# Optimization experiments

Measured on AMD Instinct MI355X. Metric: run time of the kernel, lower is better.

## Reference

```python
import jax, jax.numpy as jnp
import numpy as np

B=8; C=2; H=256; W=64; PH=4; PW=4; HP=H//PH; WP=W//PW; N=HP*WP
HID=1024; NH=16; HD=HID//NH; DEPTH=8; FFN=int(int(HID*4)*2/3); TDIM=256; OUT=PH*PW*C
EPS=1e-6


def _rmsnorm(x, w):
    return x * jax.lax.rsqrt(jnp.mean(x*x, -1, keepdims=True) + EPS) * w


def _modulate(x, shift, scale):
    return x * (1.0 + scale[:, None, :]) + shift[:, None, :]


def _rotate_half(x):
    x1 = x[..., 0::2]
    x2 = x[..., 1::2]
    return jnp.stack([-x2, x1], axis=-1).reshape(x.shape)


def _rope_tables():
    # 2D axial RoPE (EVA VisionRotaryEmbeddingFast style), dim per axis = HD//2
    dim = HD // 2
    freqs = 1.0 / (10000.0 ** (np.arange(0, dim, 2, dtype=np.float32) / dim))
    fh = np.repeat(np.outer(np.arange(HP, dtype=np.float32), freqs), 2, axis=-1)  # [HP,dim]
    fw = np.repeat(np.outer(np.arange(WP, dtype=np.float32), freqs), 2, axis=-1)  # [WP,dim]
    f = np.concatenate([np.broadcast_to(fh[:, None, :], (HP, WP, dim)),
                        np.broadcast_to(fw[None, :, :], (HP, WP, dim))], -1).reshape(N, HD)
    return jnp.asarray(np.cos(f)), jnp.asarray(np.sin(f))


def _sincos_1d(dim, pos):
    omega = np.arange(dim // 2, dtype=np.float32) / (dim / 2.0)
    omega = 1.0 / 10000.0 ** omega
    out = np.einsum('n,d->nd', pos.reshape(-1).astype(np.float32), omega)
    return np.concatenate([np.sin(out), np.cos(out)], -1)


def _pos_embed():
    gw, gh = np.meshgrid(np.arange(WP), np.arange(HP))  # row-major (HP, WP) grids
    emb = np.concatenate([_sincos_1d(HID // 2, gw), _sincos_1d(HID // 2, gh)], -1)
    return jnp.asarray(emb, dtype=jnp.float32)  # [N, HID]


_COS, _SIN = _rope_tables()
_POS = _pos_embed()


def _timestep_emb(t):
    half = TDIM // 2
    freqs = jnp.exp(-jnp.log(jnp.float32(10000.0)) * jnp.arange(half, dtype=jnp.float32) / half)
    args = t[:, None] * freqs[None]
    return jnp.concatenate([jnp.cos(args), jnp.sin(args)], -1)


def setup_inputs() -> dict:
    key = jax.random.key(0)
    ks = iter(jax.random.split(key, 16))
    def w(shape, s=0.02):
        return jax.random.normal(next(ks), shape, dtype=jnp.float32) * s
    return {
        'x': jax.random.normal(next(ks), (B, C, H, W), dtype=jnp.float32),
        't': jax.random.uniform(next(ks), (B,), dtype=jnp.float32) * 1000.0,
        'patch_w': w((HID, C, PH, PW)), 'patch_b': jnp.zeros((HID,), jnp.float32),
        't_w': w((HID, TDIM)), 't_b': jnp.zeros((HID,), jnp.float32),
        'norm1_w': jnp.ones((DEPTH, HID), jnp.float32),
        'qkv_w': w((DEPTH, 3 * HID, HID)), 'qkv_b': jnp.zeros((DEPTH, 3 * HID), jnp.float32),
        'qn_w': jnp.ones((DEPTH, HD), jnp.float32), 'kn_w': jnp.ones((DEPTH, HD), jnp.float32),
        'proj_w': w((DEPTH, HID, HID)), 'proj_b': jnp.zeros((DEPTH, HID), jnp.float32),
        'norm2_w': jnp.ones((DEPTH, HID), jnp.float32),
        'w12_w': w((DEPTH, 2 * FFN, HID)), 'w12_b': jnp.zeros((DEPTH, 2 * FFN), jnp.float32),
        'w3_w': w((DEPTH, HID, FFN)), 'w3_b': jnp.zeros((DEPTH, HID), jnp.float32),
        'ada_w': w((DEPTH, 6 * HID, HID)), 'ada_b': jnp.zeros((DEPTH, 6 * HID), jnp.float32),
        'fnorm_w': jnp.ones((HID,), jnp.float32),
        'flin_w': w((OUT, HID)), 'flin_b': jnp.zeros((OUT,), jnp.float32),
        'fada_w': w((2 * HID, HID)), 'fada_b': jnp.zeros((2 * HID,), jnp.float32),
    }


def reference(x, t, patch_w, patch_b, t_w, t_b, norm1_w, qkv_w, qkv_b, qn_w, kn_w,
              proj_w, proj_b, norm2_w, w12_w, w12_b, w3_w, w3_b, ada_w, ada_b,
              fnorm_w, flin_w, flin_b, fada_w, fada_b):
    # timestep embedding -> c : [B, HID]
    c = _timestep_emb(t) @ t_w.T + t_b
    cs = jax.nn.silu(c)
    # patch embed (conv stride==kernel == patchify + matmul)
    xp = x.reshape(B, C, HP, PH, WP, PW)
    h = jnp.einsum('bchpwq,ocpq->bhwo', xp, patch_w).reshape(B, N, HID) + patch_b
    h = h + _POS[None]
    scale = 1.0 / np.sqrt(HD)
    for d in range(DEPTH):
        ada = cs @ ada_w[d].T + ada_b[d]
        sm, scm, gm, sp, scp, gp = jnp.split(ada, 6, axis=-1)
        hn = _modulate(_rmsnorm(h, norm1_w[d]), sm, scm)
        qkv = (hn @ qkv_w[d].T + qkv_b[d]).reshape(B, N, 3, NH, HD).transpose(2, 0, 3, 1, 4)
        q, k, v = qkv[0], qkv[1], qkv[2]  # [B, NH, N, HD]
        q = _rmsnorm(q, qn_w[d]) 
        k = _rmsnorm(k, kn_w[d])
        q = q * _COS + _rotate_half(q) * _SIN
        k = k * _COS + _rotate_half(k) * _SIN
        attn = jax.nn.softmax(jnp.einsum('bhqd,bhkd->bhqk', q, k) * scale, axis=-1)
        o = jnp.einsum('bhqk,bhkd->bqhd', attn, v).reshape(B, N, HID)
        o = o @ proj_w[d].T + proj_b[d]
        h = h + gm[:, None, :] * o
        hn = _modulate(_rmsnorm(h, norm2_w[d]), sp, scp)
        x12 = hn @ w12_w[d].T + w12_b[d]
        x1, x2 = jnp.split(x12, 2, axis=-1)
        h = h + gp[:, None, :] * ((jax.nn.silu(x1) * x2) @ w3_w[d].T + w3_b[d])
    fsh, fsc = jnp.split(cs @ fada_w.T + fada_b, 2, axis=-1)
    h = _modulate(_rmsnorm(h, fnorm_w), fsh, fsc) @ flin_w.T + flin_b  # [B, N, OUT]
    y = h.reshape(B, HP, WP, PH, PW, C)
    return jnp.einsum('nhwpqc->nchpwq', y).reshape(B, C, H, W)
```

## Files before the change

### kernel.cpp

```cpp
#include <hip/hip_runtime.h>
#include <stdint.h>

typedef __bf16 bf16;
typedef __attribute__((ext_vector_type(8))) __bf16 bf16x8;
typedef __attribute__((ext_vector_type(4))) float floatx4;

#define NTOK   1024
#define TOKS   8192
#define HID_   1024
#define FFN_   2730
#define FFNP   2752
#define X12N   5460

#define EPI_BF16  0
#define EPI_QKV   1
#define EPI_RESID 2

__global__ __launch_bounds__(256) void conv_bf16(const float* __restrict__ in, bf16* __restrict__ out, int n)
{
    const int i = (blockIdx.x * 256 + threadIdx.x) * 4;
    if (i >= n) return;
    const float4 v = *(const float4*)(in + i);
    out[i + 0] = (bf16)v.x; out[i + 1] = (bf16)v.y;
    out[i + 2] = (bf16)v.z; out[i + 3] = (bf16)v.w;
}

__global__ void conv_pad_w3(const float* __restrict__ w3, bf16* __restrict__ w3p)
{
    const int kk = blockIdx.x * 256 + threadIdx.x;
    const int row = blockIdx.y;
    if (kk >= FFNP) return;
    w3p[(size_t)row * FFNP + kk] = (kk < FFN_) ? (bf16)w3[(size_t)row * FFN_ + kk] : (bf16)0.f;
}

__global__ __launch_bounds__(256) void gemm_bt(
    const bf16* __restrict__ A, const bf16* __restrict__ Bm, const float* __restrict__ bias,
    int K, int Nreal, int epi,
    bf16* __restrict__ outb, int ldo,
    bf16* __restrict__ qo, bf16* __restrict__ ko, bf16* __restrict__ vo,
    float* __restrict__ hres, const float* __restrict__ gate, int gstride)
{
    __shared__ __align__(16) bf16 As[128 * 32];
    __shared__ __align__(16) bf16 Bs[128 * 32];
    const int t    = threadIdx.x;
    const int M0   = blockIdx.y * 128;
    const int N0   = blockIdx.x * 128;
    const int lane = t & 63;
    const int w    = t >> 6;
    const int wr   = (w >> 1) * 64, wc = (w & 1) * 64;
    const int quad = lane >> 4, r16 = lane & 15;
    const int sr   = t >> 2;
    const int sk   = (t & 3) * 8;
    const int Nlast = Nreal - 1;

    floatx4 acc[4][4];
    const floatx4 zero = {0.f, 0.f, 0.f, 0.f};
    #pragma unroll
    for (int i = 0; i < 4; i++)
        #pragma unroll
        for (int j = 0; j < 4; j++) acc[i][j] = zero;

    for (int k0 = 0; k0 < K; k0 += 32) {
        const bf16* ga0 = A + (size_t)(M0 + sr) * K + k0 + sk;
        const bf16* ga1 = A + (size_t)(M0 + sr + 64) * K + k0 + sk;
        int n0c = N0 + sr;      if (n0c > Nlast) n0c = Nlast;
        int n1c = N0 + sr + 64; if (n1c > Nlast) n1c = Nlast;
        const bf16* gb0 = Bm + (size_t)n0c * K + k0 + sk;
        const bf16* gb1 = Bm + (size_t)n1c * K + k0 + sk;
        __builtin_amdgcn_global_load_lds((const __attribute__((address_space(1))) void*)ga0,
            (__attribute__((address_space(3))) void*)(As + t * 8), 16, 0, 0);
        __builtin_amdgcn_global_load_lds((const __attribute__((address_space(1))) void*)ga1,
            (__attribute__((address_space(3))) void*)(As + (t + 256) * 8), 16, 0, 0);
        __builtin_amdgcn_global_load_lds((const __attribute__((address_space(1))) void*)gb0,
            (__attribute__((address_space(3))) void*)(Bs + t * 8), 16, 0, 0);
        __builtin_amdgcn_global_load_lds((const __attribute__((address_space(1))) void*)gb1,
            (__attribute__((address_space(3))) void*)(Bs + (t + 256) * 8), 16, 0, 0);
        __syncthreads();
        bf16x8 af[4], bfv[4];
        #pragma unroll
        for (int i = 0; i < 4; i++) af[i]  = *(const bf16x8*)(As + (wr + i * 16 + r16) * 32 + quad * 8);
        #pragma unroll
        for (int j = 0; j < 4; j++) bfv[j] = *(const bf16x8*)(Bs + (wc + j * 16 + r16) * 32 + quad * 8);
        #pragma unroll
        for (int i = 0; i < 4; i++)
            #pragma unroll
            for (int j = 0; j < 4; j++)
                acc[i][j] = __builtin_amdgcn_mfma_f32_16x16x32_bf16(af[i], bfv[j], acc[i][j], 0, 0, 0);
        __syncthreads();
    }

    #pragma unroll
    for (int i = 0; i < 4; i++) {
        const int rbase = M0 + wr + i * 16 + quad * 4;
        #pragma unroll
        for (int j = 0; j < 4; j++) {
            const int col = N0 + wc + j * 16 + r16;
            if (col >= Nreal) continue;
            const float bv = bias[col];
            if (epi == EPI_BF16) {
                #pragma unroll
                for (int rr = 0; rr < 4; rr++) {
                    const int row = rbase + rr;
                    outb[(size_t)row * ldo + col] = (bf16)(acc[i][j][rr] + bv);
                }
            } else if (epi == EPI_QKV) {
                const int s = col >> 10, hh = (col >> 6) & 15, dd = col & 63;
                #pragma unroll
                for (int rr = 0; rr < 4; rr++) {
                    const int row = rbase + rr;
                    const int b = row >> 10, n = row & 1023;
                    const float vv = acc[i][j][rr] + bv;
                    if (s == 0)      qo[((size_t)(b * 16 + hh) * 1024 + n) * 64 + dd] = (bf16)vv;
                    else if (s == 1) ko[((size_t)(b * 16 + hh) * 1024 + n) * 64 + dd] = (bf16)vv;
                    else             vo[((size_t)(b * 16 + hh) * 64 + dd) * 1024 + n] = (bf16)vv;
                }
            } else {
                #pragma unroll
                for (int rr = 0; rr < 4; rr++) {
                    const int row = rbase + rr;
                    const int b = row >> 10;
                    hres[(size_t)row * 1024 + col] += gate[(size_t)b * gstride + col] * (acc[i][j][rr] + bv);
                }
            }
        }
    }
}

__global__ __launch_bounds__(256) void small_gemm(
    const float* __restrict__ Aws, const float* __restrict__ t_in,
    const float* __restrict__ W, const float* __restrict__ bias,
    float* __restrict__ out, int N, int K, int mode, int dosilu)
{
    const int w = threadIdx.x >> 6, lane = threadIdx.x & 63;
    const int col = blockIdx.x * 4 + w;
    float acc[8];
    #pragma unroll
    for (int bb = 0; bb < 8; bb++) acc[bb] = 0.f;
    float tb[8];
    if (mode == 1) {
        #pragma unroll
        for (int bb = 0; bb < 8; bb++) tb[bb] = t_in[bb];
    }
    for (int kk = lane; kk < K; kk += 64) {
        const float wv = W[(size_t)col * K + kk];
        if (mode == 1) {
            const float f = __expf(-(float)(kk & 127) * (9.21034037198f / 128.f));
            #pragma unroll
            for (int bb = 0; bb < 8; bb++) {
                const float arg = tb[bb] * f;
                const float e = (kk < 128) ? cosf(arg) : sinf(arg);
                acc[bb] += e * wv;
            }
        } else {
            #pragma unroll
            for (int bb = 0; bb < 8; bb++) acc[bb] += Aws[(size_t)bb * 1024 + kk] * wv;
        }
    }
    #pragma unroll
    for (int bb = 0; bb < 8; bb++) {
        float v2 = acc[bb];
        #pragma unroll
        for (int off = 32; off; off >>= 1) v2 += __shfl_xor(v2, off, 64);
        acc[bb] = v2;
    }
    if (lane == 0) {
        const float bv = bias[col];
        #pragma unroll
        for (int bb = 0; bb < 8; bb++) {
            float vv = acc[bb] + bv;
            if (dosilu) vv = vv / (1.f + __expf(-vv));
            out[(size_t)bb * N + col] = vv;
        }
    }
}

__global__ __launch_bounds__(256) void patch_embed(
    const float* __restrict__ x, const float* __restrict__ pw, const float* __restrict__ pb,
    float* __restrict__ h)
{
    __shared__ float xs[32];
    const int row = blockIdx.x, t = threadIdx.x;
    const int b = row >> 10, n = row & 1023;
    const int hp = n >> 4, wp = n & 15;
    if (t < 32) {
        const int c = t >> 4, ph = (t >> 2) & 3, pq = t & 3;
        xs[t] = x[((size_t)(b * 2 + c) * 256 + hp * 4 + ph) * 64 + wp * 4 + pq];
    }
    __syncthreads();
    #pragma unroll
    for (int rep = 0; rep < 4; rep++) {
        const int o = t + rep * 256;
        const float* wrow = pw + (size_t)o * 32;
        float acc = pb[o];
        #pragma unroll
        for (int e = 0; e < 32; e++) acc += xs[e] * wrow[e];
        const int seg = o >> 8, oo = o & 255;
        const float om = __expf(-(float)oo * (9.21034037198f / 256.f));
        const float pos = (seg < 2) ? (float)wp : (float)hp;
        const float arg = pos * om;
        const float pe = ((seg & 1) == 0) ? sinf(arg) : cosf(arg);
        h[(size_t)row * 1024 + o] = acc + pe;
    }
}

__global__ __launch_bounds__(256) void norm_mod(
    const float* __restrict__ h, const float* __restrict__ w,
    const float* __restrict__ ada, int sh_off, int sc_off, int stride,
    bf16* __restrict__ out)
{
    __shared__ float red[4];
    const int row = blockIdx.x, t = threadIdx.x;
    const int b = row >> 10;
    const float4 xv = ((const float4*)(h + (size_t)row * 1024))[t];
    float ss = xv.x * xv.x + xv.y * xv.y + xv.z * xv.z + xv.w * xv.w;
    #pragma unroll
    for (int off = 32; off; off >>= 1) ss += __shfl_xor(ss, off, 64);
    if ((t & 63) == 0) red[t >> 6] = ss;
    __syncthreads();
    const float total = red[0] + red[1] + red[2] + red[3];
    const float rms = rsqrtf(total * (1.f / 1024.f) + 1e-6f);
    const float* sh = ada + (size_t)b * stride + sh_off;
    const float* sc = ada + (size_t)b * stride + sc_off;
    const float vals[4] = {xv.x, xv.y, xv.z, xv.w};
    #pragma unroll
    for (int e = 0; e < 4; e++) {
        const int c2 = t * 4 + e;
        const float vv = vals[e] * rms * w[c2] * (1.f + sc[c2]) + sh[c2];
        out[(size_t)row * 1024 + c2] = (bf16)vv;
    }
}

__global__ __launch_bounds__(64) void rope_qk(
    bf16* __restrict__ q, bf16* __restrict__ k,
    const float* __restrict__ qw, const float* __restrict__ kw)
{
    const int n = blockIdx.x, bh = blockIdx.y, d = threadIdx.x;
    const size_t idx = ((size_t)bh * 1024 + n) * 64 + d;
    const float qv = (float)q[idx], kv = (float)k[idx];
    float sq = qv * qv, sk = kv * kv;
    #pragma unroll
    for (int off = 32; off; off >>= 1) { sq += __shfl_xor(sq, off, 64); sk += __shfl_xor(sk, off, 64); }
    const float rq = rsqrtf(sq * (1.f / 64.f) + 1e-6f);
    const float rk = rsqrtf(sk * (1.f / 64.f) + 1e-6f);
    const float qn = qv * rq * qw[d];
    const float kn = kv * rk * kw[d];
    const int j = (d & 31) >> 1;
    const float freq = __expf(-(float)j * (9.21034037198f / 16.f));
    const float pos = (d < 32) ? (float)(n >> 4) : (float)(n & 15);
    const float ang = pos * freq;
    const float cv = cosf(ang), sv = sinf(ang);
    const float qp = __shfl_xor(qn, 1, 64);
    const float kp = __shfl_xor(kn, 1, 64);
    const float qo = qn * cv + ((d & 1) ? qp : -qp) * sv;
    const float ko = kn * cv + ((d & 1) ? kp : -kp) * sv;
    q[idx] = (bf16)qo;
    k[idx] = (bf16)ko;
}

__global__ __launch_bounds__(256) void attn_kernel(
    const bf16* __restrict__ q, const bf16* __restrict__ k, const bf16* __restrict__ v,
    bf16* __restrict__ o)
{
    __shared__ __align__(16) bf16 Qs[2 * 64 * 32];
    __shared__ __align__(16) bf16 Ks[2 * 64 * 32];
    __shared__ __align__(16) bf16 Vt[2 * 64 * 32];
    __shared__ __align__(16) bf16 Pw[4 * 16 * 80];
    const int t = threadIdx.x;
    const int l = t & 63, wq = t >> 6;
    const int quad = l >> 4, r16 = l & 15;
    const int qt = blockIdx.x, bh = blockIdx.y;
    const int b = bh >> 4, hh = bh & 15;

    #pragma unroll
    for (int m = 0; m < 2; m++) {
        const bf16* g = q + ((size_t)bh * 1024 + qt * 64 + wq * 16 + (l >> 2)) * 64 + m * 32 + (l & 3) * 8;
        __builtin_amdgcn_global_load_lds((const __attribute__((address_space(1))) void*)g,
            (__attribute__((address_space(3))) void*)(Qs + m * 2048 + wq * 16 * 32 + l * 8), 16, 0, 0);
    }
    __syncthreads();
    bf16x8 afq[2];
    #pragma unroll
    for (int h2 = 0; h2 < 2; h2++)
        afq[h2] = *(const bf16x8*)(Qs + h2 * 2048 + (wq * 16 + r16) * 32 + quad * 8);

    float m_r[4], l_r[4];
    floatx4 oacc[4];
    const floatx4 zero = {0.f, 0.f, 0.f, 0.f};
    #pragma unroll
    for (int rr = 0; rr < 4; rr++) { m_r[rr] = -1e30f; l_r[rr] = 0.f; }
    #pragma unroll
    for (int jd = 0; jd < 4; jd++) oacc[jd] = zero;

    bf16* Pme = Pw + wq * 16 * 80;

    for (int kt = 0; kt < 16; kt++) {
        __syncthreads();
        #pragma unroll
        for (int m = 0; m < 2; m++) {
            const bf16* gk = k + ((size_t)bh * 1024 + kt * 64 + wq * 16 + (l >> 2)) * 64 + m * 32 + (l & 3) * 8;
            __builtin_amdgcn_global_load_lds((const __attribute__((address_space(1))) void*)gk,
                (__attribute__((address_space(3))) void*)(Ks + m * 2048 + wq * 16 * 32 + l * 8), 16, 0, 0);
            const bf16* gv = v + ((size_t)bh * 64 + wq * 16 + (l >> 2)) * 1024 + kt * 64 + m * 32 + (l & 3) * 8;
            __builtin_amdgcn_global_load_lds((const __attribute__((address_space(1))) void*)gv,
                (__attribute__((address_space(3))) void*)(Vt + m * 2048 + wq * 16 * 32 + l * 8), 16, 0, 0);
        }
        __syncthreads();

        floatx4 s[4];
        #pragma unroll
        for (int j = 0; j < 4; j++) {
            bf16x8 b0 = *(const bf16x8*)(Ks + 0 * 2048 + (j * 16 + r16) * 32 + quad * 8);
            bf16x8 b1 = *(const bf16x8*)(Ks + 1 * 2048 + (j * 16 + r16) * 32 + quad * 8);
            s[j] = __builtin_amdgcn_mfma_f32_16x16x32_bf16(afq[0], b0, zero, 0, 0, 0);
            s[j] = __builtin_amdgcn_mfma_f32_16x16x32_bf16(afq[1], b1, s[j], 0, 0, 0);
        }
        float alpha[4];
        #pragma unroll
        for (int rr = 0; rr < 4; rr++) {
            float mx = fmaxf(fmaxf(s[0][rr], s[1][rr]), fmaxf(s[2][rr], s[3][rr])) * 0.125f;
            #pragma unroll
            for (int off2 = 1; off2 < 16; off2 <<= 1) mx = fmaxf(mx, __shfl_xor(mx, off2, 64));
            const float mn = fmaxf(m_r[rr], mx);
            float ps = 0.f;
            #pragma unroll
            for (int j = 0; j < 4; j++) {
                const float e = __expf(s[j][rr] * 0.125f - mn);
                s[j][rr] = e; ps += e;
            }
            #pragma unroll
            for (int off2 = 1; off2 < 16; off2 <<= 1) ps += __shfl_xor(ps, off2, 64);
            alpha[rr] = __expf(m_r[rr] - mn);
            l_r[rr] = l_r[rr] * alpha[rr] + ps;
            m_r[rr] = mn;
        }
        #pragma unroll
        for (int j = 0; j < 4; j++)
            #pragma unroll
            for (int rr = 0; rr < 4; rr++)
                Pme[(quad * 4 + rr) * 80 + j * 16 + r16] = (bf16)s[j][rr];
        __asm__ volatile("s_waitcnt lgkmcnt(0)" ::: "memory");
        bf16x8 afp[2];
        #pragma unroll
        for (int st = 0; st < 2; st++)
            afp[st] = *(const bf16x8*)(Pme + r16 * 80 + st * 32 + quad * 8);
        #pragma unroll
        for (int jd = 0; jd < 4; jd++)
            #pragma unroll
            for (int rr = 0; rr < 4; rr++) oacc[jd][rr] *= alpha[rr];
        #pragma unroll
        for (int jd = 0; jd < 4; jd++) {
            bf16x8 b0 = *(const bf16x8*)(Vt + 0 * 2048 + (jd * 16 + r16) * 32 + quad * 8);
            bf16x8 b1 = *(const bf16x8*)(Vt + 1 * 2048 + (jd * 16 + r16) * 32 + quad * 8);
            oacc[jd] = __builtin_amdgcn_mfma_f32_16x16x32_bf16(afp[0], b0, oacc[jd], 0, 0, 0);
            oacc[jd] = __builtin_amdgcn_mfma_f32_16x16x32_bf16(afp[1], b1, oacc[jd], 0, 0, 0);
        }
    }
    #pragma unroll
    for (int rr = 0; rr < 4; rr++) {
        const float inv = 1.f / l_r[rr];
        const size_t base = ((size_t)b * 1024 + qt * 64 + wq * 16 + quad * 4 + rr) * 1024 + hh * 64;
        #pragma unroll
        for (int jd = 0; jd < 4; jd++)
            o[base + jd * 16 + r16] = (bf16)(oacc[jd][rr] * inv);
    }
}

__global__ void swiglu_kernel(const bf16* __restrict__ x12, bf16* __restrict__ g)
{
    const int kk = blockIdx.x * 256 + threadIdx.x;
    const int row = blockIdx.y;
    if (kk >= FFNP) return;
    float gv = 0.f;
    if (kk < FFN_) {
        const float a  = (float)x12[(size_t)row * X12N + kk];
        const float b2 = (float)x12[(size_t)row * X12N + FFN_ + kk];
        gv = a * b2 / (1.f + __expf(-a));
    }
    g[(size_t)row * FFNP + kk] = (bf16)gv;
}

__global__ __launch_bounds__(256) void final_head(
    const bf16* __restrict__ hn, const float* __restrict__ fw, const float* __restrict__ fb,
    float* __restrict__ out)
{
    __shared__ float hs[1024];
    const int row = blockIdx.x, t = threadIdx.x;
    #pragma unroll
    for (int r = 0; r < 4; r++) hs[t + r * 256] = (float)hn[(size_t)row * 1024 + t + r * 256];
    __syncthreads();
    const int o = t >> 3, s = t & 7;
    float acc = 0.f;
    const float* wr = fw + (size_t)o * 1024 + s * 128;
    const float* hb = hs + s * 128;
    for (int e = 0; e < 128; e++) acc += hb[e] * wr[e];
    #pragma unroll
    for (int off = 1; off < 8; off <<= 1) acc += __shfl_xor(acc, off, 64);
    if (s == 0) {
        acc += fb[o];
        const int b = row >> 10, n = row & 1023;
        const int hp = n >> 4, wp = n & 15;
        const int ph = o >> 3, pw = (o >> 1) & 3, c = o & 1;
        out[((size_t)(b * 2 + c) * 256 + hp * 4 + ph) * 64 + wp * 4 + pw] = acc;
    }
}

extern "C" void kernel_launch(void* const* d_in, const int* in_sizes, int n_in,
                              void* d_out, int out_size, void* d_ws, size_t ws_size,
                              hipStream_t stream)
{
    const float* x       = (const float*)d_in[0];
    const float* t_in    = (const float*)d_in[1];
    const float* patch_w = (const float*)d_in[2];
    const float* patch_b = (const float*)d_in[3];
    const float* t_w     = (const float*)d_in[4];
    const float* t_b     = (const float*)d_in[5];
    const float* norm1_w = (const float*)d_in[6];
    const float* qkv_w   = (const float*)d_in[7];
    const float* qkv_b   = (const float*)d_in[8];
    const float* qn_w    = (const float*)d_in[9];
    const float* kn_w    = (const float*)d_in[10];
    const float* proj_w  = (const float*)d_in[11];
    const float* proj_b  = (const float*)d_in[12];
    const float* norm2_w = (const float*)d_in[13];
    const float* w12_w   = (const float*)d_in[14];
    const float* w12_b   = (const float*)d_in[15];
    const float* w3_w    = (const float*)d_in[16];
    const float* w3_b    = (const float*)d_in[17];
    const float* ada_w   = (const float*)d_in[18];
    const float* ada_b   = (const float*)d_in[19];
    const float* fnorm_w = (const float*)d_in[20];
    const float* flin_w  = (const float*)d_in[21];
    const float* flin_b  = (const float*)d_in[22];
    const float* fada_w  = (const float*)d_in[23];
    const float* fada_b  = (const float*)d_in[24];

    char* ws = (char*)d_ws;
    size_t off = 0;
    auto alloc = [&](size_t nbytes) { char* p = ws + off; off += (nbytes + 255) & ~(size_t)255; return p; };
    float* h     = (float*)alloc((size_t)TOKS * 1024 * 4);
    float* cs    = (float*)alloc(8 * 1024 * 4);
    float* ada   = (float*)alloc(8 * 6144 * 4);
    float* fada  = (float*)alloc(8 * 2048 * 4);
    bf16*  hn    = (bf16*)alloc((size_t)TOKS * 1024 * 2);
    char*  U1    =         alloc((size_t)TOKS * X12N * 2);
    bf16*  qb    = (bf16*)U1;
    bf16*  kb    = qb + (size_t)TOKS * 1024;
    bf16*  vb    = kb + (size_t)TOKS * 1024;
    bf16*  ob    = vb + (size_t)TOKS * 1024;
    bf16*  x12   = (bf16*)U1;
    bf16*  g     = (bf16*)alloc((size_t)TOKS * FFNP * 2);
    bf16*  wqkvb = (bf16*)alloc((size_t)3072 * 1024 * 2);
    bf16*  wprjb = (bf16*)alloc((size_t)1024 * 1024 * 2);
    bf16*  w12b  = (bf16*)alloc((size_t)X12N * 1024 * 2);
    bf16*  w3p   = (bf16*)alloc((size_t)1024 * FFNP * 2);
    (void)ws_size; (void)in_sizes; (void)n_in; (void)out_size;

    small_gemm<<<dim3(1024 / 4), 256, 0, stream>>>(nullptr, t_in, t_w, t_b, cs, 1024, 256, 1, 1);
    patch_embed<<<dim3(TOKS), 256, 0, stream>>>(x, patch_w, patch_b, h);

    for (int d = 0; d < 8; d++) {
        small_gemm<<<dim3(6144 / 4), 256, 0, stream>>>(cs, nullptr,
            ada_w + (size_t)d * 6144 * 1024, ada_b + (size_t)d * 6144, ada, 6144, 1024, 0, 0);
        norm_mod<<<dim3(TOKS), 256, 0, stream>>>(h, norm1_w + (size_t)d * 1024, ada, 0, 1024, 6144, hn);
        conv_bf16<<<dim3(3072 * 1024 / 4 / 256), 256, 0, stream>>>(qkv_w + (size_t)d * 3072 * 1024, wqkvb, 3072 * 1024);
        gemm_bt<<<dim3(3072 / 128, 64), 256, 0, stream>>>(hn,
            wqkvb, qkv_b + (size_t)d * 3072, 1024, 3072, EPI_QKV,
            nullptr, 0, qb, kb, vb, nullptr, nullptr, 0);
        rope_qk<<<dim3(1024, 128), 64, 0, stream>>>(qb, kb, qn_w + (size_t)d * 64, kn_w + (size_t)d * 64);
        attn_kernel<<<dim3(16, 128), 256, 0, stream>>>(qb, kb, vb, ob);
        conv_bf16<<<dim3(1024 * 1024 / 4 / 256), 256, 0, stream>>>(proj_w + (size_t)d * 1024 * 1024, wprjb, 1024 * 1024);
        gemm_bt<<<dim3(1024 / 128, 64), 256, 0, stream>>>(ob,
            wprjb, proj_b + (size_t)d * 1024, 1024, 1024, EPI_RESID,
            nullptr, 0, nullptr, nullptr, nullptr, h, ada + 2048, 6144);
        norm_mod<<<dim3(TOKS), 256, 0, stream>>>(h, norm2_w + (size_t)d * 1024, ada, 3072, 4096, 6144, hn);
        conv_bf16<<<dim3(X12N * 1024 / 4 / 256), 256, 0, stream>>>(w12_w + (size_t)d * X12N * 1024, w12b, X12N * 1024);
        gemm_bt<<<dim3(43, 64), 256, 0, stream>>>(hn,
            w12b, w12_b + (size_t)d * X12N, 1024, X12N, EPI_BF16,
            x12, X12N, nullptr, nullptr, nullptr, nullptr, nullptr, 0);
        swiglu_kernel<<<dim3(11, TOKS), 256, 0, stream>>>(x12, g);
        conv_pad_w3<<<dim3(11, 1024), 256, 0, stream>>>(w3_w + (size_t)d * 1024 * FFN_, w3p);
        gemm_bt<<<dim3(1024 / 128, 64), 256, 0, stream>>>(g,
            w3p, w3_b + (size_t)d * 1024, FFNP, 1024, EPI_RESID,
            nullptr, 0, nullptr, nullptr, nullptr, h, ada + 5120, 6144);
    }

    small_gemm<<<dim3(2048 / 4), 256, 0, stream>>>(cs, nullptr, fada_w, fada_b, fada, 2048, 1024, 0, 0);
    norm_mod<<<dim3(TOKS), 256, 0, stream>>>(h, fnorm_w, fada, 0, 1024, 2048, hn);
    final_head<<<dim3(TOKS), 256, 0, stream>>>(hn, flin_w, flin_b, (float*)d_out);
}
```

Measured before the change: 5.539 ms.

## Replace GEMM with 256x256 double-buffered swizzled LDS pipeline kernel

Replaces the 128x128 single-buffered GEMM with a 256x256-tile, 512-thread kernel. It double-buffers 64-wide K tiles in LDS with XOR swizzling, interleaves global-to-LDS staging with MFMA phases, raises wave priority during compute, and remaps workgroups across XCDs. FFN padding grows to a multiple of 128 so K tiles divide evenly. rope_qk also now packs four tokens per block. The larger tiles cut global traffic per FLOP and hide load latency, but the QKV/proj/w3 grids become small (384 or 128 blocks), which risks occupancy loss on a 256-CU part.

```diff
diff --git a/kernel.cpp b/kernel.cpp
--- a/kernel.cpp
+++ b/kernel.cpp
@@ -9,7 +9,7 @@
 #define TOKS   8192
 #define HID_   1024
 #define FFN_   2730
-#define FFNP   2752
+#define FFNP   2816
 #define X12N   5460
 
 #define EPI_BF16  0
@@ -33,93 +33,163 @@
     w3p[(size_t)row * FFNP + kk] = (kk < FFN_) ? (bf16)w3[(size_t)row * FFN_ + kk] : (bf16)0.f;
 }
 
-__global__ __launch_bounds__(256) void gemm_bt(
+#define GLL(src, dst) __builtin_amdgcn_global_load_lds( \
+    (const __attribute__((address_space(1))) void*)(src), \
+    (__attribute__((address_space(3))) void*)(dst), 16, 0, 0)
+
+#define STAGE_A(bufi, hi, tile) GLL(pA[hi] + (size_t)(tile) * 64, As + (bufi) * 16384 + ((hi) * 512 + t) * 8)
+#define STAGE_B(bufi, hi, tile) GLL(pB[hi] + (size_t)(tile) * 64, Bs + (bufi) * 16384 + ((hi) * 512 + t) * 8)
+
+#define LOADA(bufi, qm) { _Pragma("unroll") for (int mf = 0; mf < 4; mf++) { \
+    a[mf][0] = *(const bf16x8*)(As + (bufi) * 16384 + (qm) * 8192 + arow64 + mf * 1024 + swz0); \
+    a[mf][1] = *(const bf16x8*)(As + (bufi) * 16384 + (qm) * 8192 + arow64 + mf * 1024 + swz1); } }
+
+#define LOADB(bufi, qn) { _Pragma("unroll") for (int nf = 0; nf < 2; nf++) { \
+    b[nf][0] = *(const bf16x8*)(Bs + (bufi) * 16384 + (qn) * 8192 + brow64 + nf * 1024 + swz0); \
+    b[nf][1] = *(const bf16x8*)(Bs + (bufi) * 16384 + (qn) * 8192 + brow64 + nf * 1024 + swz1); } }
+
+#define MM(qm, qn) { _Pragma("unroll") for (int mf = 0; mf < 4; mf++) \
+    _Pragma("unroll") for (int nf = 0; nf < 2; nf++) { \
+    acc[qm][qn][mf][nf] = __builtin_amdgcn_mfma_f32_16x16x32_bf16(a[mf][0], b[nf][0], acc[qm][qn][mf][nf], 0, 0, 0); \
+    acc[qm][qn][mf][nf] = __builtin_amdgcn_mfma_f32_16x16x32_bf16(a[mf][1], b[nf][1], acc[qm][qn][mf][nf], 0, 0, 0); } }
+
+#define PHTAIL(...) { __builtin_amdgcn_s_barrier(); \
+    asm volatile("s_waitcnt lgkmcnt(0)" ::: "memory"); \
+    __builtin_amdgcn_sched_barrier(0); \
+    __builtin_amdgcn_s_setprio(1); __VA_ARGS__; __builtin_amdgcn_s_setprio(0); \
+    __builtin_amdgcn_s_barrier(); }
+
+__global__ __launch_bounds__(512, 2) void gemm256(
     const bf16* __restrict__ A, const bf16* __restrict__ Bm, const float* __restrict__ bias,
     int K, int Nreal, int epi,
     bf16* __restrict__ outb, int ldo,
     bf16* __restrict__ qo, bf16* __restrict__ ko, bf16* __restrict__ vo,
     float* __restrict__ hres, const float* __restrict__ gate, int gstride)
 {
-    __shared__ __align__(16) bf16 As[128 * 32];
-    __shared__ __align__(16) bf16 Bs[128 * 32];
-    const int t    = threadIdx.x;
-    const int M0   = blockIdx.y * 128;
-    const int N0   = blockIdx.x * 128;
-    const int lane = t & 63;
-    const int w    = t >> 6;
-    const int wr   = (w >> 1) * 64, wc = (w & 1) * 64;
+    __shared__ __align__(16) bf16 As[2 * 16384];
+    __shared__ __align__(16) bf16 Bs[2 * 16384];
+    const int t = threadIdx.x;
+
+    const int gx = gridDim.x;
+    int wg = blockIdx.y * gx + blockIdx.x;
+    {
+        const int nwg = gx * gridDim.y;
+        const int q8 = nwg >> 3, r8 = nwg & 7;
+        const int xcd = wg & 7, pos = wg >> 3;
+        wg = (xcd < r8 ? xcd * (q8 + 1) : r8 * (q8 + 1) + (xcd - r8) * q8) + pos;
+    }
+    const int M0 = (wg / gx) * 256, N0 = (wg % gx) * 256;
+    const int Nlast = Nreal - 1;
+
+    const int lane = t & 63, w = t >> 6;
+    const int wm = w >> 2, wn = w & 3;
     const int quad = lane >> 4, r16 = lane & 15;
-    const int sr   = t >> 2;
-    const int sk   = (t & 3) * 8;
-    const int Nlast = Nreal - 1;
-
-    floatx4 acc[4][4];
+
+    const int rS = t >> 3;
+    const int cswS = (t & 7) ^ (rS & 7);
+    const bf16* pA[4]; const bf16* pB[4];
+    #pragma unroll
+    for (int hi = 0; hi < 4; hi++) {
+        pA[hi] = A + (size_t)(M0 + hi * 64 + rS) * K + cswS * 8;
+        int nb = N0 + hi * 64 + rS; if (nb > Nlast) nb = Nlast;
+        pB[hi] = Bm + (size_t)nb * K + cswS * 8;
+    }
+
+    const int arow64 = (wm * 64 + r16) * 64;
+    const int brow64 = (wn * 32 + r16) * 64;
+    const int swz0 = ((0 * 4 + quad) ^ (r16 & 7)) * 8;
+    const int swz1 = ((1 * 4 + quad) ^ (r16 & 7)) * 8;
+
+    floatx4 acc[2][2][4][2];
     const floatx4 zero = {0.f, 0.f, 0.f, 0.f};
     #pragma unroll
-    for (int i = 0; i < 4; i++)
-        #pragma unroll
-        for (int j = 0; j < 4; j++) acc[i][j] = zero;
-
-    for (int k0 = 0; k0 < K; k0 += 32) {
-        const bf16* ga0 = A + (size_t)(M0 + sr) * K + k0 + sk;
-        const bf16* ga1 = A + (size_t)(M0 + sr + 64) * K + k0 + sk;
-        int n0c = N0 + sr;      if (n0c > Nlast) n0c = Nlast;
-        int n1c = N0 + sr + 64; if (n1c > Nlast) n1c = Nlast;
-        const bf16* gb0 = Bm + (size_t)n0c * K + k0 + sk;
-        const bf16* gb1 = Bm + (size_t)n1c * K + k0 + sk;
-        __builtin_amdgcn_global_load_lds((const __attribute__((address_space(1))) void*)ga0,
-            (__attribute__((address_space(3))) void*)(As + t * 8), 16, 0, 0);
-        __builtin_amdgcn_global_load_lds((const __attribute__((address_space(1))) void*)ga1,
-            (__attribute__((address_space(3))) void*)(As + (t + 256) * 8), 16, 0, 0);
-        __builtin_amdgcn_global_load_lds((const __attribute__((address_space(1))) void*)gb0,
-            (__attribute__((address_space(3))) void*)(Bs + t * 8), 16, 0, 0);
-        __builtin_amdgcn_global_load_lds((const __attribute__((address_space(1))) void*)gb1,
-            (__attribute__((address_space(3))) void*)(Bs + (t + 256) * 8), 16, 0, 0);
-        __syncthreads();
-        bf16x8 af[4], bfv[4];
-        #pragma unroll
-        for (int i = 0; i < 4; i++) af[i]  = *(const bf16x8*)(As + (wr + i * 16 + r16) * 32 + quad * 8);
-        #pragma unroll
-        for (int j = 0; j < 4; j++) bfv[j] = *(const bf16x8*)(Bs + (wc + j * 16 + r16) * 32 + quad * 8);
-        #pragma unroll
-        for (int i = 0; i < 4; i++)
-            #pragma unroll
-            for (int j = 0; j < 4; j++)
-                acc[i][j] = __builtin_amdgcn_mfma_f32_16x16x32_bf16(af[i], bfv[j], acc[i][j], 0, 0, 0);
-        __syncthreads();
-    }
-
-    #pragma unroll
-    for (int i = 0; i < 4; i++) {
-        const int rbase = M0 + wr + i * 16 + quad * 4;
-        #pragma unroll
-        for (int j = 0; j < 4; j++) {
-            const int col = N0 + wc + j * 16 + r16;
+    for (int i0 = 0; i0 < 2; i0++)
+        #pragma unroll
+        for (int i1 = 0; i1 < 2; i1++)
+            #pragma unroll
+            for (int i2 = 0; i2 < 4; i2++)
+                #pragma unroll
+                for (int i3 = 0; i3 < 2; i3++) acc[i0][i1][i2][i3] = zero;
+    bf16x8 a[4][2], b[2][2];
+
+    const int NT = K >> 6;
+    const int NI = NT >> 1;
+
+    STAGE_A(0, 0, 0); STAGE_A(0, 1, 0);
+    STAGE_B(0, 0, 0); STAGE_B(0, 1, 0);
+    STAGE_B(0, 2, 0); STAGE_B(0, 3, 0);
+    STAGE_A(0, 2, 0); STAGE_A(0, 3, 0);
+    STAGE_A(1, 0, 1); STAGE_A(1, 1, 1);
+    STAGE_B(1, 0, 1); STAGE_B(1, 1, 1);
+    asm volatile("s_waitcnt vmcnt(4)" ::: "memory");
+    __builtin_amdgcn_s_barrier();
+
+    for (int it = 0; it < NI; ++it) {
+        const bool last = (it == NI - 1);
+        const int to = 2 * it + 1, te2 = 2 * it + 2, to2 = 2 * it + 3;
+        LOADA(0, 0); LOADB(0, 0);
+        STAGE_A(1, 2, to); STAGE_A(1, 3, to);
+        PHTAIL(MM(0, 0));
+        LOADB(0, 1);
+        STAGE_B(1, 2, to); STAGE_B(1, 3, to);
+        PHTAIL(MM(0, 1));
+        LOADA(0, 1); LOADB(0, 0);
+        if (!last) { STAGE_A(0, 0, te2); STAGE_A(0, 1, te2); }
+        PHTAIL(MM(1, 0));
+        LOADB(0, 1);
+        if (!last) { STAGE_B(0, 0, te2); STAGE_B(0, 1, te2);
+                     asm volatile("s_waitcnt vmcnt(4)" ::: "memory"); }
+        else       { asm volatile("s_waitcnt vmcnt(0)" ::: "memory"); }
+        PHTAIL(MM(1, 1));
+        LOADA(1, 0); LOADB(1, 0);
+        if (!last) { STAGE_A(0, 2, te2); STAGE_A(0, 3, te2); }
+        PHTAIL(MM(0, 0));
+        LOADB(1, 1);
+        if (!last) { STAGE_B(0, 2, te2); STAGE_B(0, 3, te2); }
+        PHTAIL(MM(0, 1));
+        LOADA(1, 1); LOADB(1, 0);
+        if (!last) { STAGE_A(1, 0, to2); STAGE_A(1, 1, to2); }
+        PHTAIL(MM(1, 0));
+        LOADB(1, 1);
+        if (!last) { STAGE_B(1, 0, to2); STAGE_B(1, 1, to2);
+                     asm volatile("s_waitcnt vmcnt(4)" ::: "memory"); }
+        PHTAIL(MM(1, 1));
+    }
+
+    #pragma unroll
+    for (int qm = 0; qm < 2; qm++)
+    #pragma unroll
+    for (int mf = 0; mf < 4; mf++) {
+        const int rbase = M0 + qm * 128 + wm * 64 + mf * 16 + quad * 4;
+        #pragma unroll
+        for (int qn = 0; qn < 2; qn++)
+        #pragma unroll
+        for (int nf = 0; nf < 2; nf++) {
+            const int col = N0 + qn * 128 + wn * 32 + nf * 16 + r16;
             if (col >= Nreal) continue;
             const float bv = bias[col];
+            const floatx4 av = acc[qm][qn][mf][nf];
             if (epi == EPI_BF16) {
                 #pragma unroll
-                for (int rr = 0; rr < 4; rr++) {
-                    const int row = rbase + rr;
-                    outb[(size_t)row * ldo + col] = (bf16)(acc[i][j][rr] + bv);
-                }
+                for (int rr = 0; rr < 4; rr++)
+                    outb[(size_t)(rbase + rr) * ldo + col] = (bf16)(av[rr] + bv);
             } else if (epi == EPI_QKV) {
                 const int s = col >> 10, hh = (col >> 6) & 15, dd = col & 63;
                 #pragma unroll
                 for (int rr = 0; rr < 4; rr++) {
                     const int row = rbase + rr;
-                    const int b = row >> 10, n = row & 1023;
-                    const float vv = acc[i][j][rr] + bv;
-                    if (s == 0)      qo[((size_t)(b * 16 + hh) * 1024 + n) * 64 + dd] = (bf16)vv;
-                    else if (s == 1) ko[((size_t)(b * 16 + hh) * 1024 + n) * 64 + dd] = (bf16)vv;
-                    else             vo[((size_t)(b * 16 + hh) * 64 + dd) * 1024 + n] = (bf16)vv;
+                    const int bb = row >> 10, n = row & 1023;
+                    const float vv = av[rr] + bv;
+                    if (s == 0)      qo[((size_t)(bb * 16 + hh) * 1024 + n) * 64 + dd] = (bf16)vv;
+                    else if (s == 1) ko[((size_t)(bb * 16 + hh) * 1024 + n) * 64 + dd] = (bf16)vv;
+                    else             vo[((size_t)(bb * 16 + hh) * 64 + dd) * 1024 + n] = (bf16)vv;
                 }
             } else {
                 #pragma unroll
                 for (int rr = 0; rr < 4; rr++) {
                     const int row = rbase + rr;
-                    const int b = row >> 10;
-                    hres[(size_t)row * 1024 + col] += gate[(size_t)b * gstride + col] * (acc[i][j][rr] + bv);
+                    const int bb = row >> 10;
+                    hres[(size_t)row * 1024 + col] += gate[(size_t)bb * gstride + col] * (av[rr] + bv);
                 }
             }
         }
@@ -230,11 +300,12 @@
     }
 }
 
-__global__ __launch_bounds__(64) void rope_qk(
+__global__ __launch_bounds__(256) void rope_qk(
     bf16* __restrict__ q, bf16* __restrict__ k,
     const float* __restrict__ qw, const float* __restrict__ kw)
 {
-    const int n = blockIdx.x, bh = blockIdx.y, d = threadIdx.x;
+    const int n = blockIdx.x * 4 + (threadIdx.x >> 6);
+    const int bh = blockIdx.y, d = threadIdx.x & 63;
     const size_t idx = ((size_t)bh * 1024 + n) * 64 + d;
     const float qv = (float)q[idx], kv = (float)k[idx];
     float sq = qv * qv, sk = kv * kv;
@@ -463,23 +534,23 @@
             ada_w + (size_t)d * 6144 * 1024, ada_b + (size_t)d * 6144, ada, 6144, 1024, 0, 0);
         norm_mod<<<dim3(TOKS), 256, 0, stream>>>(h, norm1_w + (size_t)d * 1024, ada, 0, 1024, 6144, hn);
         conv_bf16<<<dim3(3072 * 1024 / 4 / 256), 256, 0, stream>>>(qkv_w + (size_t)d * 3072 * 1024, wqkvb, 3072 * 1024);
-        gemm_bt<<<dim3(3072 / 128, 64), 256, 0, stream>>>(hn,
+        gemm256<<<dim3(3072 / 256, 32), 512, 0, stream>>>(hn,
             wqkvb, qkv_b + (size_t)d * 3072, 1024, 3072, EPI_QKV,
             nullptr, 0, qb, kb, vb, nullptr, nullptr, 0);
-        rope_qk<<<dim3(1024, 128), 64, 0, stream>>>(qb, kb, qn_w + (size_t)d * 64, kn_w + (size_t)d * 64);
+        rope_qk<<<dim3(256, 128), 256, 0, stream>>>(qb, kb, qn_w + (size_t)d * 64, kn_w + (size_t)d * 64);
         attn_kernel<<<dim3(16, 128), 256, 0, stream>>>(qb, kb, vb, ob);
         conv_bf16<<<dim3(1024 * 1024 / 4 / 256), 256, 0, stream>>>(proj_w + (size_t)d * 1024 * 1024, wprjb, 1024 * 1024);
-        gemm_bt<<<dim3(1024 / 128, 64), 256, 0, stream>>>(ob,
+        gemm256<<<dim3(1024 / 256, 32), 512, 0, stream>>>(ob,
             wprjb, proj_b + (size_t)d * 1024, 1024, 1024, EPI_RESID,
             nullptr, 0, nullptr, nullptr, nullptr, h, ada + 2048, 6144);
         norm_mod<<<dim3(TOKS), 256, 0, stream>>>(h, norm2_w + (size_t)d * 1024, ada, 3072, 4096, 6144, hn);
         conv_bf16<<<dim3(X12N * 1024 / 4 / 256), 256, 0, stream>>>(w12_w + (size_t)d * X12N * 1024, w12b, X12N * 1024);
-        gemm_bt<<<dim3(43, 64), 256, 0, stream>>>(hn,
+        gemm256<<<dim3((X12N + 255) / 256, 32), 512, 0, stream>>>(hn,
             w12b, w12_b + (size_t)d * X12N, 1024, X12N, EPI_BF16,
             x12, X12N, nullptr, nullptr, nullptr, nullptr, nullptr, 0);
-        swiglu_kernel<<<dim3(11, TOKS), 256, 0, stream>>>(x12, g);
-        conv_pad_w3<<<dim3(11, 1024), 256, 0, stream>>>(w3_w + (size_t)d * 1024 * FFN_, w3p);
-        gemm_bt<<<dim3(1024 / 128, 64), 256, 0, stream>>>(g,
+        swiglu_kernel<<<dim3(FFNP / 256, TOKS), 256, 0, stream>>>(x12, g);
+        conv_pad_w3<<<dim3(FFNP / 256, 1024), 256, 0, stream>>>(w3_w + (size_t)d * 1024 * FFN_, w3p);
+        gemm256<<<dim3(1024 / 256, 32), 512, 0, stream>>>(g,
             w3p, w3_b + (size_t)d * 1024, FFNP, 1024, EPI_RESID,
             nullptr, 0, nullptr, nullptr, nullptr, h, ada + 5120, 6144);
     }
```

After: 5.558 ms. Within noise of the previous version (+0.3%).
